# Kernel tuning notes

Measured on AMD Instinct MI355X. Metric: run time of the kernel, lower is better.

The kernel has to match this reference:

```python
import jax, jax.numpy as jnp
import numpy as np

B, T, D, K = 16, 1024, 256, 1024

def setup_inputs() -> dict:
    key = jax.random.key(0)
    k1, k2 = jax.random.split(key)
    x = jax.random.normal(k1, (B, T, D), dtype=jnp.float32)
    codebook = jax.random.normal(k2, (K, D), dtype=jnp.float32)
    precision = jnp.ones((1,), dtype=jnp.float32)
    return {"x": x, "codebook": codebook, "precision": precision}

def reference(x, codebook, precision):
    # score[b,t,k] = -precision * ||x[b,t] - codebook[k]||^2
    x_sq = jnp.sum(x * x, axis=-1, keepdims=True)            # [B,T,1]
    c_sq = jnp.sum(codebook * codebook, axis=-1)             # [K]
    xc = jnp.einsum('btd,kd->btk', x, codebook)              # [B,T,K]
    dist_sq = x_sq - 2.0 * xc + c_sq                         # [B,T,K]
    return -precision[0] * dist_sq
```

## Files before the change

### kernel.cpp

```cpp
#include <hip/hip_runtime.h>
#include <hip/hip_bf16.h>
#include <cstdint>

#define M_ROWS 16384
#define D_DIM  256
#define K_ROWS 1024

typedef __bf16 bf16x8 __attribute__((ext_vector_type(8)));
typedef __bf16 bf16x4 __attribute__((ext_vector_type(4)));
typedef float  f32x4  __attribute__((ext_vector_type(4)));

__global__ __launch_bounds__(256) void prep_kernel(
    const float* __restrict__ x, const float* __restrict__ cb,
    __bf16* __restrict__ xbf, __bf16* __restrict__ cbf,
    float* __restrict__ xsq, float* __restrict__ csq)
{
  const int row = blockIdx.x * 4 + (threadIdx.x >> 6);
  const int l   = threadIdx.x & 63;

  const float* src;
  __bf16* dst;
  float* nrm;
  if (row < M_ROWS) {
    src = x   + (size_t)row * D_DIM;
    dst = xbf + (size_t)row * D_DIM;
    nrm = xsq + row;
  } else {
    const int r = row - M_ROWS;
    src = cb  + (size_t)r * D_DIM;
    dst = cbf + (size_t)r * D_DIM;
    nrm = csq + r;
  }

  const float4 v = reinterpret_cast<const float4*>(src)[l];
  float s = v.x * v.x + v.y * v.y + v.z * v.z + v.w * v.w;

  bf16x4 h;
  h[0] = (__bf16)v.x; h[1] = (__bf16)v.y; h[2] = (__bf16)v.z; h[3] = (__bf16)v.w;
  *reinterpret_cast<bf16x4*>(dst + l * 4) = h;

  #pragma unroll
  for (int o = 32; o > 0; o >>= 1) s += __shfl_xor(s, o);
  if (l == 0) *nrm = s;
}

__global__ __launch_bounds__(256) void gemm_kernel(
    const __bf16* __restrict__ xbf, const __bf16* __restrict__ cbf,
    const float* __restrict__ xsq, const float* __restrict__ csq,
    const float* __restrict__ prec, float* __restrict__ out)
{
  __shared__ __bf16 At[128 * 64];
  __shared__ __bf16 Bt[128 * 64];

  const int tid = threadIdx.x;
  const int w   = tid >> 6;
  const int l   = tid & 63;
  const int wr  = w >> 1;
  const int wc  = w & 1;

  const int bx   = blockIdx.x;
  const int tile = (bx & 7) * 128 + (bx >> 3);
  const int tr   = tile >> 3;
  const int tc   = tile & 7;
  const int row0 = tr * 128;
  const int col0 = tc * 128;

  const int srow = tid >> 3;
  const int sg   = tid & 7;
  const int swg  = (sg ^ (srow & 7)) * 16;
  const __bf16* gA = xbf + (size_t)(row0 + srow) * D_DIM + sg * 8;
  const __bf16* gB = cbf + (size_t)(col0 + srow) * D_DIM + sg * 8;
  char* const wA = (char*)At + srow * 128 + swg;
  char* const wB = (char*)Bt + srow * 128 + swg;

  f32x4 acc[4][4] = {};

  const int lr = l & 15;
  const int lk = l >> 4;

  bf16x8 ra[4], rb[4];
  #pragma unroll
  for (int n = 0; n < 4; ++n) {
    ra[n] = *reinterpret_cast<const bf16x8*>(gA + (size_t)(n * 32) * D_DIM);
    rb[n] = *reinterpret_cast<const bf16x8*>(gB + (size_t)(n * 32) * D_DIM);
  }

  #pragma unroll
  for (int t = 0; t < 4; ++t) {
    #pragma unroll
    for (int n = 0; n < 4; ++n) {
      *reinterpret_cast<bf16x8*>(wA + n * 4096) = ra[n];
      *reinterpret_cast<bf16x8*>(wB + n * 4096) = rb[n];
    }
    __syncthreads();

    if (t < 3) {
      const int k0 = (t + 1) * 64;
      #pragma unroll
      for (int n = 0; n < 4; ++n) {
        ra[n] = *reinterpret_cast<const bf16x8*>(gA + (size_t)(n * 32) * D_DIM + k0);
        rb[n] = *reinterpret_cast<const bf16x8*>(gB + (size_t)(n * 32) * D_DIM + k0);
      }
    }

    #pragma unroll
    for (int ks = 0; ks < 2; ++ks) {
      bf16x8 af[4], bfm[4];
      #pragma unroll
      for (int f = 0; f < 4; ++f) {
        const int rar = wr * 64 + f * 16 + lr;
        af[f] = *reinterpret_cast<const bf16x8*>(
            (const char*)At + rar * 128 + ((ks * 64 + lk * 16) ^ ((rar & 7) << 4)));
        const int rbr = wc * 64 + f * 16 + lr;
        bfm[f] = *reinterpret_cast<const bf16x8*>(
            (const char*)Bt + rbr * 128 + ((ks * 64 + lk * 16) ^ ((rbr & 7) << 4)));
      }
      #pragma unroll
      for (int i = 0; i < 4; ++i)
        #pragma unroll
        for (int j = 0; j < 4; ++j)
          acc[i][j] = __builtin_amdgcn_mfma_f32_16x16x32_bf16(bfm[j], af[i], acc[i][j], 0, 0, 0);
    }
    __syncthreads();
  }

  const float p = prec[0];
  #pragma unroll
  for (int i = 0; i < 4; ++i) {
    const int rowg = row0 + wr * 64 + i * 16 + lr;
    const float xs = xsq[rowg];
    float* orow = out + (size_t)rowg * K_ROWS;
    #pragma unroll
    for (int j = 0; j < 4; ++j) {
      const int colg = col0 + wc * 64 + j * 16 + lk * 4;
      const f32x4 cs = *reinterpret_cast<const f32x4*>(&csq[colg]);
      f32x4 v;
      #pragma unroll
      for (int r = 0; r < 4; ++r)
        v[r] = -p * (xs - 2.0f * acc[i][j][r] + cs[r]);
      *reinterpret_cast<f32x4*>(&orow[colg]) = v;
    }
  }
}

extern "C" void kernel_launch(void* const* d_in, const int* in_sizes, int n_in,
                              void* d_out, int out_size, void* d_ws, size_t ws_size,
                              hipStream_t stream) {
  const float* x    = (const float*)d_in[0];
  const float* cb   = (const float*)d_in[1];
  const float* prec = (const float*)d_in[2];
  float* out = (float*)d_out;

  char* ws = (char*)d_ws;
  __bf16* xbf = (__bf16*)ws;
  __bf16* cbf = (__bf16*)(ws + 8388608);
  float*  xsq = (float*)(ws + 8912896);
  float*  csq = (float*)(ws + 8978432);

  prep_kernel<<<(M_ROWS + K_ROWS) / 4, 256, 0, stream>>>(x, cb, xbf, cbf, xsq, csq);
  gemm_kernel<<<(M_ROWS / 128) * (K_ROWS / 128), 256, 0, stream>>>(xbf, cbf, xsq, csq, prec, out);
}
```

Baseline: 33.61 us.

## Fuse bf16 conversion and norm computation into the GEMM kernel

```diff
diff --git a/kernel.cpp b/kernel.cpp
--- a/kernel.cpp
+++ b/kernel.cpp
@@ -7,50 +7,37 @@
 #define K_ROWS 1024
 
 typedef __bf16 bf16x8 __attribute__((ext_vector_type(8)));
-typedef __bf16 bf16x4 __attribute__((ext_vector_type(4)));
 typedef float  f32x4  __attribute__((ext_vector_type(4)));
 
-__global__ __launch_bounds__(256) void prep_kernel(
+
+#define LOADCVT(k0)                                                            \
+  do {                                                                         \
+    _Pragma("unroll")                                                          \
+    for (int n = 0; n < 4; ++n) {                                              \
+      const f32x4 a0 = *reinterpret_cast<const f32x4*>(gA + (size_t)(n * 32) * D_DIM + (k0));     \
+      const f32x4 a1 = *reinterpret_cast<const f32x4*>(gA + (size_t)(n * 32) * D_DIM + (k0) + 4); \
+      const f32x4 b0 = *reinterpret_cast<const f32x4*>(gB + (size_t)(n * 32) * D_DIM + (k0));     \
+      const f32x4 b1 = *reinterpret_cast<const f32x4*>(gB + (size_t)(n * 32) * D_DIM + (k0) + 4); \
+      _Pragma("unroll")                                                        \
+      for (int j = 0; j < 4; ++j) {                                            \
+        sumA[n] += a0[j] * a0[j] + a1[j] * a1[j];                              \
+        sumB[n] += b0[j] * b0[j] + b1[j] * b1[j];                              \
+        pa[n][j]     = (__bf16)a0[j];                                          \
+        pa[n][j + 4] = (__bf16)a1[j];                                          \
+        pb[n][j]     = (__bf16)b0[j];                                          \
+        pb[n][j + 4] = (__bf16)b1[j];                                          \
+      }                                                                        \
+    }                                                                          \
+  } while (0)
+
+__global__ __launch_bounds__(256) void fused_kernel(
     const float* __restrict__ x, const float* __restrict__ cb,
-    __bf16* __restrict__ xbf, __bf16* __restrict__ cbf,
-    float* __restrict__ xsq, float* __restrict__ csq)
-{
-  const int row = blockIdx.x * 4 + (threadIdx.x >> 6);
-  const int l   = threadIdx.x & 63;
-
-  const float* src;
-  __bf16* dst;
-  float* nrm;
-  if (row < M_ROWS) {
-    src = x   + (size_t)row * D_DIM;
-    dst = xbf + (size_t)row * D_DIM;
-    nrm = xsq + row;
-  } else {
-    const int r = row - M_ROWS;
-    src = cb  + (size_t)r * D_DIM;
-    dst = cbf + (size_t)r * D_DIM;
-    nrm = csq + r;
-  }
-
-  const float4 v = reinterpret_cast<const float4*>(src)[l];
-  float s = v.x * v.x + v.y * v.y + v.z * v.z + v.w * v.w;
-
-  bf16x4 h;
-  h[0] = (__bf16)v.x; h[1] = (__bf16)v.y; h[2] = (__bf16)v.z; h[3] = (__bf16)v.w;
-  *reinterpret_cast<bf16x4*>(dst + l * 4) = h;
-
-  #pragma unroll
-  for (int o = 32; o > 0; o >>= 1) s += __shfl_xor(s, o);
-  if (l == 0) *nrm = s;
-}
-
-__global__ __launch_bounds__(256) void gemm_kernel(
-    const __bf16* __restrict__ xbf, const __bf16* __restrict__ cbf,
-    const float* __restrict__ xsq, const float* __restrict__ csq,
     const float* __restrict__ prec, float* __restrict__ out)
 {
   __shared__ __bf16 At[128 * 64];
   __shared__ __bf16 Bt[128 * 64];
+  __shared__ float  xsqs[128];
+  __shared__ float  csqs[128];
 
   const int tid = threadIdx.x;
   const int w   = tid >> 6;
@@ -67,41 +54,35 @@
 
   const int srow = tid >> 3;
   const int sg   = tid & 7;
-  const int swg  = (sg ^ (srow & 7)) * 16;
-  const __bf16* gA = xbf + (size_t)(row0 + srow) * D_DIM + sg * 8;
-  const __bf16* gB = cbf + (size_t)(col0 + srow) * D_DIM + sg * 8;
-  char* const wA = (char*)At + srow * 128 + swg;
-  char* const wB = (char*)Bt + srow * 128 + swg;
+  const int swb  = (sg ^ (srow & 7)) << 4;
+  const float* gA = x  + (size_t)(row0 + srow) * D_DIM + sg * 8;
+  const float* gB = cb + (size_t)(col0 + srow) * D_DIM + sg * 8;
+  char* const wAbase = (char*)At + srow * 128 + swb;
+  char* const wBbase = (char*)Bt + srow * 128 + swb;
 
-  f32x4 acc[4][4] = {};
+  const float p = prec[0];
+
+  f32x4  acc[4][4] = {};
+  float  sumA[4] = {}, sumB[4] = {};
+  bf16x8 pa[4], pb[4];
 
   const int lr = l & 15;
   const int lk = l >> 4;
 
-  bf16x8 ra[4], rb[4];
-  #pragma unroll
-  for (int n = 0; n < 4; ++n) {
-    ra[n] = *reinterpret_cast<const bf16x8*>(gA + (size_t)(n * 32) * D_DIM);
-    rb[n] = *reinterpret_cast<const bf16x8*>(gB + (size_t)(n * 32) * D_DIM);
-  }
+  LOADCVT(0);
 
   #pragma unroll
   for (int t = 0; t < 4; ++t) {
     #pragma unroll
     for (int n = 0; n < 4; ++n) {
-      *reinterpret_cast<bf16x8*>(wA + n * 4096) = ra[n];
-      *reinterpret_cast<bf16x8*>(wB + n * 4096) = rb[n];
+      *reinterpret_cast<bf16x8*>(wAbase + n * 4096) = pa[n];
+      *reinterpret_cast<bf16x8*>(wBbase + n * 4096) = pb[n];
     }
     __syncthreads();
 
-    if (t < 3) {
-      const int k0 = (t + 1) * 64;
-      #pragma unroll
-      for (int n = 0; n < 4; ++n) {
-        ra[n] = *reinterpret_cast<const bf16x8*>(gA + (size_t)(n * 32) * D_DIM + k0);
-        rb[n] = *reinterpret_cast<const bf16x8*>(gB + (size_t)(n * 32) * D_DIM + k0);
-      }
-    }
+    if (t == 0) LOADCVT(64);
+    if (t == 1) LOADCVT(128);
+    if (t == 2) LOADCVT(192);
 
     #pragma unroll
     for (int ks = 0; ks < 2; ++ks) {
@@ -124,21 +105,32 @@
     __syncthreads();
   }
 
-  const float p = prec[0];
+  #pragma unroll
+  for (int n = 0; n < 4; ++n) {
+    float a = sumA[n], b = sumB[n];
+    a += __shfl_xor(a, 1); a += __shfl_xor(a, 2); a += __shfl_xor(a, 4);
+    b += __shfl_xor(b, 1); b += __shfl_xor(b, 2); b += __shfl_xor(b, 4);
+    if (sg == 0) {
+      xsqs[n * 32 + srow] = a;
+      csqs[n * 32 + srow] = b;
+    }
+  }
+  __syncthreads();
+
   #pragma unroll
   for (int i = 0; i < 4; ++i) {
-    const int rowg = row0 + wr * 64 + i * 16 + lr;
-    const float xs = xsq[rowg];
-    float* orow = out + (size_t)rowg * K_ROWS;
+    const int rloc = wr * 64 + i * 16 + lr;
+    const float xs = xsqs[rloc];
+    float* orow = out + (size_t)(row0 + rloc) * K_ROWS + col0;
     #pragma unroll
     for (int j = 0; j < 4; ++j) {
-      const int colg = col0 + wc * 64 + j * 16 + lk * 4;
-      const f32x4 cs = *reinterpret_cast<const f32x4*>(&csq[colg]);
+      const int cloc = wc * 64 + j * 16 + lk * 4;
+      const f32x4 cs = *reinterpret_cast<const f32x4*>(&csqs[cloc]);
       f32x4 v;
       #pragma unroll
       for (int r = 0; r < 4; ++r)
         v[r] = -p * (xs - 2.0f * acc[i][j][r] + cs[r]);
-      *reinterpret_cast<f32x4*>(&orow[colg]) = v;
+      *reinterpret_cast<f32x4*>(&orow[cloc]) = v;
     }
   }
 }
@@ -151,12 +143,5 @@
   const float* prec = (const float*)d_in[2];
   float* out = (float*)d_out;
 
-  char* ws = (char*)d_ws;
-  __bf16* xbf = (__bf16*)ws;
-  __bf16* cbf = (__bf16*)(ws + 8388608);
-  float*  xsq = (float*)(ws + 8912896);
-  float*  csq = (float*)(ws + 8978432);
-
-  prep_kernel<<<(M_ROWS + K_ROWS) / 4, 256, 0, stream>>>(x, cb, xbf, cbf, xsq, csq);
-  gemm_kernel<<<(M_ROWS / 128) * (K_ROWS / 128), 256, 0, stream>>>(xbf, cbf, xsq, csq, prec, out);
+  fused_kernel<<<(M_ROWS / 128) * (K_ROWS / 128), 256, 0, stream>>>(x, cb, prec, out);
 }
```

Measured after the change: 40.86 us. +21.6%, slower.
